# Optimization experiments

Hardware: AMD Instinct MI355X
Metric: run time of the kernel (lower is better)

Reference implementation:

```python
import math
import jax
import jax.numpy as jnp
import numpy as np

SEGMENT_SIZE = 2048   # w (init: segment_size)
DILATION_RATE = 4     # r (init: dilation_rate)
D_MODEL = 1024        # init: d_model


def _sparse_indices(n: int, w: int, r: int, head_idx: int) -> np.ndarray:
    """Static SparsifyIndices: per segment of size w, take tokens offset::r.
    Since r divides w, every segment yields exactly m=w//r indices (no -1 pad).
    Returns flat global token indices, shape (S*m,)."""
    S = n // w
    m = w // r
    off = head_idx % r
    seg_start = np.arange(S, dtype=np.int64)[:, None] * w      # (S,1)
    within = off + r * np.arange(m, dtype=np.int64)[None, :]   # (1,m)
    return (seg_start + within).reshape(-1)


def setup_inputs() -> dict:
    key = jax.random.key(0)
    x = jax.random.normal(key, (4, 8192, D_MODEL), dtype=jnp.float32)
    return {"x": x, "head_idx": 1}


def reference(x, head_idx):
    b, n0, d = x.shape
    w, r = SEGMENT_SIZE, DILATION_RATE
    pad = (-n0) % w
    if pad:
        x = jnp.pad(x, ((0, 0), (0, pad), (0, 0)))
    n = n0 + pad
    idx = _sparse_indices(n, w, r, int(head_idx))  # static, (S*m,)
    S, m = n // w, w // r

    # Gather dilated tokens per segment: (b, S, m, d)
    xg = x[:, idx, :].reshape(b, S, m, d)

    # Softmax attention within each sub-segment (q=k=v=xg)
    scores = jnp.einsum('bsid,bsjd->bsij', xg, xg) / math.sqrt(d)  # (b,S,m,m)
    probs = jax.nn.softmax(scores, axis=-1)
    att = jnp.einsum('bsij,bsjd->bsid', probs, xg).reshape(b, S * m, d)

    # MixOutputs: alpha-weighted scatter-add back to full sequence
    denoms = att.sum(-1)                                       # (b, S*m)
    denom_sums = jnp.zeros((b, n), x.dtype).at[:, idx].add(denoms)
    alphas = denoms / denom_sums[:, idx]                       # (b, S*m)
    out = jnp.zeros((b, n, d), x.dtype).at[:, idx, :].add(att * alphas[..., None])
    return out
```

## Files before the change

### kernel.cpp

```cpp
#include <hip/hip_runtime.h>
#include <hip/hip_bf16.h>


typedef __bf16 bf16_t;
typedef __bf16 bf16x8 __attribute__((ext_vector_type(8)));
typedef float floatx4 __attribute__((ext_vector_type(4)));

#define D_MODEL 1024
#define SEG_W   2048
#define RATE    4
#define M_SUB   512
#define NTOK    8192
#define NSEGT   16
#define XG_ELEMS ((long)NSEGT * M_SUB * D_MODEL)
#define QK_SCALE 0.17677669529663689f

__device__ __forceinline__ void gload16(const bf16_t* g, bf16_t* l) {
    __builtin_amdgcn_global_load_lds(
        (const __attribute__((address_space(1))) void*)g,
        (__attribute__((address_space(3))) void*)l, 16, 0, 0);
}

__global__ __launch_bounds__(256) void gather_kernel(
    const float* __restrict__ x, const int* __restrict__ hidp,
    bf16_t* __restrict__ xg, bf16_t* __restrict__ xgT)
{
    const int off = ((hidp[0] % RATE) + RATE) % RATE;
    const int bid = blockIdx.x;
    const int seg = bid >> 7;
    const int rem = bid & 127;
    const int it  = rem >> 4;
    const int dt  = rem & 15;
    const int b   = seg >> 2, s = seg & 3;

    __shared__ ushort tile[64][65];

    const int t  = threadIdx.x;
    const int r  = t >> 2;
    const int cq = (t & 3) << 4;

    union U8 { bf16x8 v; ushort u[8]; };

    {
        const int  i   = it * 64 + r;
        const long tok = (long)s * SEG_W + off + 4L * i;
        const float* src = x + ((long)b * NTOK + tok) * D_MODEL + dt * 64 + cq;
        float4 f0 = ((const float4*)src)[0];
        float4 f1 = ((const float4*)src)[1];
        float4 f2 = ((const float4*)src)[2];
        float4 f3 = ((const float4*)src)[3];
        U8 lo, hi, ls, hs;
        lo.v[0]=(bf16_t)f0.x; lo.v[1]=(bf16_t)f0.y; lo.v[2]=(bf16_t)f0.z; lo.v[3]=(bf16_t)f0.w;
        lo.v[4]=(bf16_t)f1.x; lo.v[5]=(bf16_t)f1.y; lo.v[6]=(bf16_t)f1.z; lo.v[7]=(bf16_t)f1.w;
        hi.v[0]=(bf16_t)f2.x; hi.v[1]=(bf16_t)f2.y; hi.v[2]=(bf16_t)f2.z; hi.v[3]=(bf16_t)f2.w;
        hi.v[4]=(bf16_t)f3.x; hi.v[5]=(bf16_t)f3.y; hi.v[6]=(bf16_t)f3.z; hi.v[7]=(bf16_t)f3.w;
        ls.v[0]=(bf16_t)(f0.x*QK_SCALE); ls.v[1]=(bf16_t)(f0.y*QK_SCALE);
        ls.v[2]=(bf16_t)(f0.z*QK_SCALE); ls.v[3]=(bf16_t)(f0.w*QK_SCALE);
        ls.v[4]=(bf16_t)(f1.x*QK_SCALE); ls.v[5]=(bf16_t)(f1.y*QK_SCALE);
        ls.v[6]=(bf16_t)(f1.z*QK_SCALE); ls.v[7]=(bf16_t)(f1.w*QK_SCALE);
        hs.v[0]=(bf16_t)(f2.x*QK_SCALE); hs.v[1]=(bf16_t)(f2.y*QK_SCALE);
        hs.v[2]=(bf16_t)(f2.z*QK_SCALE); hs.v[3]=(bf16_t)(f2.w*QK_SCALE);
        hs.v[4]=(bf16_t)(f3.x*QK_SCALE); hs.v[5]=(bf16_t)(f3.y*QK_SCALE);
        hs.v[6]=(bf16_t)(f3.z*QK_SCALE); hs.v[7]=(bf16_t)(f3.w*QK_SCALE);
        bf16_t* dstg = xg + ((long)seg * M_SUB + i) * D_MODEL + dt * 64 + cq;
        *(bf16x8*)(dstg)     = ls.v;
        *(bf16x8*)(dstg + 8) = hs.v;
        #pragma unroll
        for (int j = 0; j < 8; ++j) { tile[r][cq + j] = lo.u[j]; tile[r][cq + 8 + j] = hi.u[j]; }
    }
    __syncthreads();
    {
        const int dc = r;
        const int iq = cq;
        U8 o0, o1;
        #pragma unroll
        for (int j = 0; j < 8; ++j) { o0.u[j] = tile[iq + j][dc]; o1.u[j] = tile[iq + 8 + j][dc]; }
        bf16_t* dstT = xgT + ((long)seg * D_MODEL + dt * 64 + dc) * M_SUB + it * 64 + iq;
        *(bf16x8*)(dstT)     = o0.v;
        *(bf16x8*)(dstT + 8) = o1.v;
    }
}

__global__ __launch_bounds__(256) void qk_kernel(
    const bf16_t* __restrict__ xg, bf16_t* __restrict__ S)
{
    const int bid = blockIdx.x;
    const int seg = bid >> 5;
    const int mt  = (bid >> 2) & 7;
    const int nt  = bid & 3;

    const int tid  = threadIdx.x;
    const int w    = tid >> 6;
    const int lane = tid & 63;
    const int l16  = lane & 15;
    const int quad = lane >> 4;
    const int wr   = w >> 1, wc = w & 1;
    const int rowin = lane >> 3;
    const int cswz  = ((lane & 7) ^ rowin) * 8;
    const int rsw   = l16 & 7;

    __shared__ alignas(16) bf16_t As[64 * 64];
    __shared__ alignas(16) bf16_t Bs[128 * 64];

    const bf16_t* xseg = xg + (long)seg * M_SUB * D_MODEL;

    const bf16_t* ga0 = xseg + (long)(mt * 64 + w * 16 + rowin) * D_MODEL + cswz;
    const bf16_t* ga1 = ga0 + 8 * D_MODEL;
    const bf16_t* gb0 = xseg + (long)(nt * 128 + w * 32 + rowin) * D_MODEL + cswz;
    const bf16_t* gb1 = gb0 +  8 * D_MODEL;
    const bf16_t* gb2 = gb0 + 16 * D_MODEL;
    const bf16_t* gb3 = gb0 + 24 * D_MODEL;
    bf16_t* la0 = &As[(w * 16 + 0) * 64];
    bf16_t* la1 = &As[(w * 16 + 8) * 64];
    bf16_t* lb0 = &Bs[(w * 32 + 0) * 64];
    bf16_t* lb1 = &Bs[(w * 32 + 8) * 64];
    bf16_t* lb2 = &Bs[(w * 32 + 16) * 64];
    bf16_t* lb3 = &Bs[(w * 32 + 24) * 64];

    floatx4 acc[2][4];
    #pragma unroll
    for (int i = 0; i < 2; ++i)
        #pragma unroll
        for (int j = 0; j < 4; ++j) acc[i][j] = (floatx4){0.f, 0.f, 0.f, 0.f};

    for (int kk = 0; kk < D_MODEL; kk += 64) {
        __syncthreads();
        gload16(ga0 + kk, la0); gload16(ga1 + kk, la1);
        gload16(gb0 + kk, lb0); gload16(gb1 + kk, lb1);
        gload16(gb2 + kk, lb2); gload16(gb3 + kk, lb3);
        __syncthreads();

        #pragma unroll
        for (int ks = 0; ks < 2; ++ks) {
            bf16x8 Af[2], Bf[4];
            #pragma unroll
            for (int m2 = 0; m2 < 2; ++m2) {
                const int row = wr * 32 + m2 * 16 + l16;
                Af[m2] = *(const bf16x8*)&As[row * 64 + (((ks * 4 + quad) ^ rsw) * 8)];
            }
            #pragma unroll
            for (int n2 = 0; n2 < 4; ++n2) {
                const int row = wc * 64 + n2 * 16 + l16;
                Bf[n2] = *(const bf16x8*)&Bs[row * 64 + (((ks * 4 + quad) ^ rsw) * 8)];
            }
            #pragma unroll
            for (int m2 = 0; m2 < 2; ++m2)
                #pragma unroll
                for (int n2 = 0; n2 < 4; ++n2)
                    acc[m2][n2] = __builtin_amdgcn_mfma_f32_16x16x32_bf16(Af[m2], Bf[n2], acc[m2][n2], 0, 0, 0);
        }
    }

    bf16_t* Sseg = S + (long)seg * M_SUB * M_SUB;
    #pragma unroll
    for (int m2 = 0; m2 < 2; ++m2) {
        const int qrow = mt * 64 + wr * 32 + m2 * 16 + quad * 4;
        #pragma unroll
        for (int n2 = 0; n2 < 4; ++n2) {
            const int col = nt * 128 + wc * 64 + n2 * 16 + l16;
            #pragma unroll
            for (int rg = 0; rg < 4; ++rg)
                Sseg[(long)(qrow + rg) * M_SUB + col] = (bf16_t)acc[m2][n2][rg];
        }
    }
}

__global__ __launch_bounds__(256) void softmax_kernel(bf16_t* __restrict__ S)
{
    const int row  = blockIdx.x * 4 + (threadIdx.x >> 6);
    const int lane = threadIdx.x & 63;
    bf16_t* p = S + (long)row * M_SUB + lane * 8;
    bf16x8 v = *(const bf16x8*)p;
    float f[8];
    #pragma unroll
    for (int j = 0; j < 8; ++j) f[j] = (float)v[j];
    float m = f[0];
    #pragma unroll
    for (int j = 1; j < 8; ++j) m = fmaxf(m, f[j]);
    #pragma unroll
    for (int d = 1; d < 64; d <<= 1) m = fmaxf(m, __shfl_xor(m, d, 64));
    float sum = 0.f;
    #pragma unroll
    for (int j = 0; j < 8; ++j) { f[j] = __expf(f[j] - m); sum += f[j]; }
    #pragma unroll
    for (int d = 1; d < 64; d <<= 1) sum += __shfl_xor(sum, d, 64);
    const float inv = 1.0f / sum;
    #pragma unroll
    for (int j = 0; j < 8; ++j) v[j] = (bf16_t)(f[j] * inv);
    *(bf16x8*)p = v;
}

__global__ __launch_bounds__(256) void pv_kernel(
    const bf16_t* __restrict__ P, const bf16_t* __restrict__ xgT,
    const int* __restrict__ hidp, float* __restrict__ out)
{
    const int off = ((hidp[0] % RATE) + RATE) % RATE;
    const int bid = blockIdx.x;
    const int seg = bid >> 6;
    const int mt  = (bid >> 3) & 7;
    const int nt  = bid & 7;
    const int b   = seg >> 2, s = seg & 3;

    const int tid  = threadIdx.x;
    const int w    = tid >> 6;
    const int lane = tid & 63;
    const int l16  = lane & 15;
    const int quad = lane >> 4;
    const int wr   = w >> 1, wc = w & 1;
    const int rowin = lane >> 3;
    const int cswz  = ((lane & 7) ^ rowin) * 8;
    const int rsw   = l16 & 7;

    __shared__ alignas(16) bf16_t Stile[64 * 512];
    __shared__ alignas(16) bf16_t Bs[128 * 64];

    const bf16_t* Prow0 = P + (long)seg * M_SUB * M_SUB + (long)(mt * 64) * M_SUB;
    #pragma unroll
    for (int i = 0; i < 16; ++i) {
        const int row = w * 16 + i;
        const bf16_t* g = Prow0 + (long)row * M_SUB + ((lane ^ (i & 7)) * 8);
        gload16(g, &Stile[row * 512]);
    }

    const bf16_t* Bseg = xgT + (long)seg * D_MODEL * M_SUB + (long)nt * 128 * M_SUB;
    const bf16_t* gb0 = Bseg + (long)(w * 32 + rowin) * M_SUB + cswz;
    const bf16_t* gb1 = gb0 +  8 * M_SUB;
    const bf16_t* gb2 = gb0 + 16 * M_SUB;
    const bf16_t* gb3 = gb0 + 24 * M_SUB;
    bf16_t* lb0 = &Bs[(w * 32 + 0) * 64];
    bf16_t* lb1 = &Bs[(w * 32 + 8) * 64];
    bf16_t* lb2 = &Bs[(w * 32 + 16) * 64];
    bf16_t* lb3 = &Bs[(w * 32 + 24) * 64];

    floatx4 acc[2][4];
    #pragma unroll
    for (int i = 0; i < 2; ++i)
        #pragma unroll
        for (int j = 0; j < 4; ++j) acc[i][j] = (floatx4){0.f, 0.f, 0.f, 0.f};

    for (int kk = 0; kk < M_SUB; kk += 64) {
        __syncthreads();
        gload16(gb0 + kk, lb0); gload16(gb1 + kk, lb1);
        gload16(gb2 + kk, lb2); gload16(gb3 + kk, lb3);
        __syncthreads();

        const int kchunk = kk >> 3;
        #pragma unroll
        for (int ks = 0; ks < 2; ++ks) {
            bf16x8 Af[2], Bf[4];
            #pragma unroll
            for (int m2 = 0; m2 < 2; ++m2) {
                const int row = wr * 32 + m2 * 16 + l16;
                Af[m2] = *(const bf16x8*)&Stile[row * 512 + (kchunk | ((ks * 4 + quad) ^ rsw)) * 8];
            }
            #pragma unroll
            for (int n2 = 0; n2 < 4; ++n2) {
                const int row = wc * 64 + n2 * 16 + l16;
                Bf[n2] = *(const bf16x8*)&Bs[row * 64 + (((ks * 4 + quad) ^ rsw) * 8)];
            }
            #pragma unroll
            for (int m2 = 0; m2 < 2; ++m2)
                #pragma unroll
                for (int n2 = 0; n2 < 4; ++n2)
                    acc[m2][n2] = __builtin_amdgcn_mfma_f32_16x16x32_bf16(Af[m2], Bf[n2], acc[m2][n2], 0, 0, 0);
        }
    }

    float* obase = out + (long)b * NTOK * D_MODEL;
    #pragma unroll
    for (int m2 = 0; m2 < 2; ++m2) {
        const int qrow0 = mt * 64 + wr * 32 + m2 * 16 + quad * 4;
        #pragma unroll
        for (int rg = 0; rg < 4; ++rg) {
            const long tok = (long)s * SEG_W + off + 4L * (qrow0 + rg);
            float* orow = obase + tok * D_MODEL;
            #pragma unroll
            for (int n2 = 0; n2 < 4; ++n2) {
                const int d = nt * 128 + wc * 64 + n2 * 16 + l16;
                __builtin_nontemporal_store(acc[m2][n2][rg], &orow[d]);
            }
        }
    }

    {
        const floatx4 z = {0.f, 0.f, 0.f, 0.f};
        const int zr = tid >> 5;
        const int zc = tid & 31;
        #pragma unroll 4
        for (int p = 0; p < 24; ++p) {
            const int j = p * 8 + zr;
            const int q = j / 3, e = j % 3;
            const int delta = e + (e >= off ? 1 : 0);
            const long tok = (long)s * SEG_W + 4L * (mt * 64 + q) + delta;
            float* dst = obase + tok * D_MODEL + nt * 128 + zc * 4;
            __builtin_nontemporal_store(z, (floatx4*)dst);
        }
    }
}

extern "C" void kernel_launch(void* const* d_in, const int* in_sizes, int n_in,
                              void* d_out, int out_size, void* d_ws, size_t ws_size,
                              hipStream_t stream) {
    const float* x   = (const float*)d_in[0];
    const int*   hid = (const int*)d_in[1];
    float*       out = (float*)d_out;
    bf16_t* xg  = (bf16_t*)d_ws;
    bf16_t* xgT = xg + XG_ELEMS;
    bf16_t* S   = xgT + XG_ELEMS;

    gather_kernel<<<dim3(2048), dim3(256), 0, stream>>>(x, hid, xg, xgT);
    qk_kernel<<<dim3(512), dim3(256), 0, stream>>>(xg, S);
    softmax_kernel<<<dim3(2048), dim3(256), 0, stream>>>(S);
    pv_kernel<<<dim3(1024), dim3(256), 0, stream>>>(S, xgT, hid, out);
}
```

Before: 251.9 us.

## Use 8-wave blocks for QK and PV, tiling PV's A operand in K

The QK kernel moves from 4 to 8 waves per block, with each wave computing a 32x32 sub-tile instead of 32x64, so the block tile stays 64x128 with more waves to hide latency. The PV kernel switches from 64x128 to 128x128 output tiles with 512 threads. It also streams the probability tile in 64-wide K chunks instead of preloading a full 64x512 row block into LDS, which shrinks shared memory use and raises reuse of the xgT tile. The trade-off is fewer PV blocks, 512 instead of 1024, which may lower parallelism and occupancy.

```diff
diff --git a/kernel.cpp b/kernel.cpp
--- a/kernel.cpp
+++ b/kernel.cpp
@@ -81,7 +81,7 @@
     }
 }
 
-__global__ __launch_bounds__(256) void qk_kernel(
+__global__ __launch_bounds__(512) void qk_kernel(
     const bf16_t* __restrict__ xg, bf16_t* __restrict__ S)
 {
     const int bid = blockIdx.x;
@@ -94,59 +94,52 @@
     const int lane = tid & 63;
     const int l16  = lane & 15;
     const int quad = lane >> 4;
-    const int wr   = w >> 1, wc = w & 1;
-    const int rowin = lane >> 3;
-    const int cswz  = ((lane & 7) ^ rowin) * 8;
-    const int rsw   = l16 & 7;
+    const int wr   = w >> 2, wc = w & 3;
+    const int row8 = lane >> 3;
+    const int cswz = ((lane & 7) ^ row8) * 8;
+    const int rsw  = l16 & 7;
 
     __shared__ alignas(16) bf16_t As[64 * 64];
     __shared__ alignas(16) bf16_t Bs[128 * 64];
 
     const bf16_t* xseg = xg + (long)seg * M_SUB * D_MODEL;
 
-    const bf16_t* ga0 = xseg + (long)(mt * 64 + w * 16 + rowin) * D_MODEL + cswz;
-    const bf16_t* ga1 = ga0 + 8 * D_MODEL;
-    const bf16_t* gb0 = xseg + (long)(nt * 128 + w * 32 + rowin) * D_MODEL + cswz;
-    const bf16_t* gb1 = gb0 +  8 * D_MODEL;
-    const bf16_t* gb2 = gb0 + 16 * D_MODEL;
-    const bf16_t* gb3 = gb0 + 24 * D_MODEL;
-    bf16_t* la0 = &As[(w * 16 + 0) * 64];
-    bf16_t* la1 = &As[(w * 16 + 8) * 64];
-    bf16_t* lb0 = &Bs[(w * 32 + 0) * 64];
-    bf16_t* lb1 = &Bs[(w * 32 + 8) * 64];
-    bf16_t* lb2 = &Bs[(w * 32 + 16) * 64];
-    bf16_t* lb3 = &Bs[(w * 32 + 24) * 64];
-
-    floatx4 acc[2][4];
+    const bf16_t* ga  = xseg + (long)(mt * 64 + w * 8 + row8) * D_MODEL + cswz;
+    const bf16_t* gb0 = xseg + (long)(nt * 128 + w * 16 + row8) * D_MODEL + cswz;
+    const bf16_t* gb1 = gb0 + 8 * D_MODEL;
+    bf16_t* la  = &As[(w * 8) * 64];
+    bf16_t* lb0 = &Bs[(w * 16 + 0) * 64];
+    bf16_t* lb1 = &Bs[(w * 16 + 8) * 64];
+
+    floatx4 acc[2][2];
     #pragma unroll
     for (int i = 0; i < 2; ++i)
         #pragma unroll
-        for (int j = 0; j < 4; ++j) acc[i][j] = (floatx4){0.f, 0.f, 0.f, 0.f};
+        for (int j = 0; j < 2; ++j) acc[i][j] = (floatx4){0.f, 0.f, 0.f, 0.f};
 
     for (int kk = 0; kk < D_MODEL; kk += 64) {
         __syncthreads();
-        gload16(ga0 + kk, la0); gload16(ga1 + kk, la1);
+        gload16(ga  + kk, la);
         gload16(gb0 + kk, lb0); gload16(gb1 + kk, lb1);
-        gload16(gb2 + kk, lb2); gload16(gb3 + kk, lb3);
         __syncthreads();
 
         #pragma unroll
         for (int ks = 0; ks < 2; ++ks) {
-            bf16x8 Af[2], Bf[4];
+            bf16x8 Af[2], Bf[2];
             #pragma unroll
             for (int m2 = 0; m2 < 2; ++m2) {
                 const int row = wr * 32 + m2 * 16 + l16;
                 Af[m2] = *(const bf16x8*)&As[row * 64 + (((ks * 4 + quad) ^ rsw) * 8)];
             }
             #pragma unroll
-            for (int n2 = 0; n2 < 4; ++n2) {
-                const int row = wc * 64 + n2 * 16 + l16;
+            for (int n2 = 0; n2 < 2; ++n2) {
+                const int row = wc * 32 + n2 * 16 + l16;
                 Bf[n2] = *(const bf16x8*)&Bs[row * 64 + (((ks * 4 + quad) ^ rsw) * 8)];
             }
             #pragma unroll
             for (int m2 = 0; m2 < 2; ++m2)
                 #pragma unroll
-                for (int n2 = 0; n2 < 4; ++n2)
+                for (int n2 = 0; n2 < 2; ++n2)
                     acc[m2][n2] = __builtin_amdgcn_mfma_f32_16x16x32_bf16(Af[m2], Bf[n2], acc[m2][n2], 0, 0, 0);
         }
     }
@@ -156,8 +149,8 @@
     for (int m2 = 0; m2 < 2; ++m2) {
         const int qrow = mt * 64 + wr * 32 + m2 * 16 + quad * 4;
         #pragma unroll
-        for (int n2 = 0; n2 < 4; ++n2) {
-            const int col = nt * 128 + wc * 64 + n2 * 16 + l16;
+        for (int n2 = 0; n2 < 2; ++n2) {
+            const int col = nt * 128 + wc * 32 + n2 * 16 + l16;
             #pragma unroll
             for (int rg = 0; rg < 4; ++rg)
                 Sseg[(long)(qrow + rg) * M_SUB + col] = (bf16_t)acc[m2][n2][rg];
@@ -190,14 +183,14 @@
     *(bf16x8*)p = v;
 }
 
-__global__ __launch_bounds__(256) void pv_kernel(
+__global__ __launch_bounds__(512) void pv_kernel(
     const bf16_t* __restrict__ P, const bf16_t* __restrict__ xgT,
     const int* __restrict__ hidp, float* __restrict__ out)
 {
     const int off = ((hidp[0] % RATE) + RATE) % RATE;
     const int bid = blockIdx.x;
-    const int seg = bid >> 6;
-    const int mt  = (bid >> 3) & 7;
+    const int seg = bid >> 5;
+    const int mt  = (bid >> 3) & 3;
     const int nt  = bid & 7;
     const int b   = seg >> 2, s = seg & 3;
 
@@ -207,30 +200,24 @@
     const int l16  = lane & 15;
     const int quad = lane >> 4;
     const int wr   = w >> 1, wc = w & 1;
-    const int rowin = lane >> 3;
-    const int cswz  = ((lane & 7) ^ rowin) * 8;
-    const int rsw   = l16 & 7;
-
-    __shared__ alignas(16) bf16_t Stile[64 * 512];
+    const int row8 = lane >> 3;
+    const int cswz = ((lane & 7) ^ row8) * 8;
+    const int rsw  = l16 & 7;
+
+    __shared__ alignas(16) bf16_t As[128 * 64];
     __shared__ alignas(16) bf16_t Bs[128 * 64];
 
-    const bf16_t* Prow0 = P + (long)seg * M_SUB * M_SUB + (long)(mt * 64) * M_SUB;
-    #pragma unroll
-    for (int i = 0; i < 16; ++i) {
-        const int row = w * 16 + i;
-        const bf16_t* g = Prow0 + (long)row * M_SUB + ((lane ^ (i & 7)) * 8);
-        gload16(g, &Stile[row * 512]);
-    }
-
+    const bf16_t* Aseg = P   + (long)seg * M_SUB * M_SUB  + (long)mt * 128 * M_SUB;
     const bf16_t* Bseg = xgT + (long)seg * D_MODEL * M_SUB + (long)nt * 128 * M_SUB;
-    const bf16_t* gb0 = Bseg + (long)(w * 32 + rowin) * M_SUB + cswz;
-    const bf16_t* gb1 = gb0 +  8 * M_SUB;
-    const bf16_t* gb2 = gb0 + 16 * M_SUB;
-    const bf16_t* gb3 = gb0 + 24 * M_SUB;
-    bf16_t* lb0 = &Bs[(w * 32 + 0) * 64];
-    bf16_t* lb1 = &Bs[(w * 32 + 8) * 64];
-    bf16_t* lb2 = &Bs[(w * 32 + 16) * 64];
-    bf16_t* lb3 = &Bs[(w * 32 + 24) * 64];
+
+    const bf16_t* ga0 = Aseg + (long)(w * 16 + row8) * M_SUB + cswz;
+    const bf16_t* ga1 = ga0 + 8 * M_SUB;
+    const bf16_t* gb0 = Bseg + (long)(w * 16 + row8) * M_SUB + cswz;
+    const bf16_t* gb1 = gb0 + 8 * M_SUB;
+    bf16_t* la0 = &As[(w * 16 + 0) * 64];
+    bf16_t* la1 = &As[(w * 16 + 8) * 64];
+    bf16_t* lb0 = &Bs[(w * 16 + 0) * 64];
+    bf16_t* lb1 = &Bs[(w * 16 + 8) * 64];
 
     floatx4 acc[2][4];
     #pragma unroll
@@ -240,18 +227,17 @@
 
     for (int kk = 0; kk < M_SUB; kk += 64) {
         __syncthreads();
+        gload16(ga0 + kk, la0); gload16(ga1 + kk, la1);
         gload16(gb0 + kk, lb0); gload16(gb1 + kk, lb1);
-        gload16(gb2 + kk, lb2); gload16(gb3 + kk, lb3);
         __syncthreads();
 
-        const int kchunk = kk >> 3;
         #pragma unroll
         for (int ks = 0; ks < 2; ++ks) {
             bf16x8 Af[2], Bf[4];
             #pragma unroll
             for (int m2 = 0; m2 < 2; ++m2) {
                 const int row = wr * 32 + m2 * 16 + l16;
-                Af[m2] = *(const bf16x8*)&Stile[row * 512 + (kchunk | ((ks * 4 + quad) ^ rsw)) * 8];
+                Af[m2] = *(const bf16x8*)&As[row * 64 + (((ks * 4 + quad) ^ rsw) * 8)];
             }
             #pragma unroll
             for (int n2 = 0; n2 < 4; ++n2) {
@@ -269,7 +255,7 @@
     float* obase = out + (long)b * NTOK * D_MODEL;
     #pragma unroll
     for (int m2 = 0; m2 < 2; ++m2) {
-        const int qrow0 = mt * 64 + wr * 32 + m2 * 16 + quad * 4;
+        const int qrow0 = mt * 128 + wr * 32 + m2 * 16 + quad * 4;
         #pragma unroll
         for (int rg = 0; rg < 4; ++rg) {
             const long tok = (long)s * SEG_W + off + 4L * (qrow0 + rg);
@@ -288,10 +274,10 @@
         const int zc = tid & 31;
         #pragma unroll 4
         for (int p = 0; p < 24; ++p) {
-            const int j = p * 8 + zr;
+            const int j = p * 16 + zr;
             const int q = j / 3, e = j % 3;
             const int delta = e + (e >= off ? 1 : 0);
-            const long tok = (long)s * SEG_W + 4L * (mt * 64 + q) + delta;
+            const long tok = (long)s * SEG_W + 4L * (mt * 128 + q) + delta;
             float* dst = obase + tok * D_MODEL + nt * 128 + zc * 4;
             __builtin_nontemporal_store(z, (floatx4*)dst);
         }
@@ -309,7 +295,7 @@
     bf16_t* S   = xgT + XG_ELEMS;
 
     gather_kernel<<<dim3(2048), dim3(256), 0, stream>>>(x, hid, xg, xgT);
-    qk_kernel<<<dim3(512), dim3(256), 0, stream>>>(xg, S);
+    qk_kernel<<<dim3(512), dim3(512), 0, stream>>>(xg, S);
     softmax_kernel<<<dim3(2048), dim3(256), 0, stream>>>(S);
-    pv_kernel<<<dim3(1024), dim3(256), 0, stream>>>(S, xgT, hid, out);
-}
+    pv_kernel<<<dim3(512), dim3(512), 0, stream>>>(S, xgT, hid, out);
+}
```

After: 250.1 us. No clear change (-0.7%).
